# Kernel optimization log

Hardware: AMD Instinct MI355X
Metric: run time of the kernel (lower is better)

Reference implementation:

```python
import jax, jax.numpy as jnp
import numpy as np

B, N, D, H = 4, 2048, 512, 8
HD = D // H


def setup_inputs() -> dict:
    key = jax.random.key(0)
    ks = jax.random.split(key, 10)
    x = jax.random.normal(ks[0], (B, N, D), dtype=jnp.float32)
    adj = (jax.random.uniform(ks[1], (N, N)) < 0.1).astype(jnp.float32)
    s = 1.0 / np.sqrt(D)
    Wq = jax.random.normal(ks[2], (D, D), dtype=jnp.float32) * s
    Wk = jax.random.normal(ks[3], (D, D), dtype=jnp.float32) * s
    Wv = jax.random.normal(ks[4], (D, D), dtype=jnp.float32) * s
    Wo = jax.random.normal(ks[5], (D, D), dtype=jnp.float32) * s
    bq = jnp.zeros((D,), jnp.float32)
    bk = jnp.zeros((D,), jnp.float32)
    bv = jnp.zeros((D,), jnp.float32)
    bo = jnp.zeros((D,), jnp.float32)
    return {"x": x, "adj": adj, "Wq": Wq, "bq": bq, "Wk": Wk, "bk": bk,
            "Wv": Wv, "bv": bv, "Wo": Wo, "bo": bo}


def reference(x, adj, Wq, bq, Wk, bk, Wv, bv, Wo, bo):
    b, n, d = x.shape
    q = (x @ Wq + bq).reshape(b, n, H, HD)
    k = (x @ Wk + bk).reshape(b, n, H, HD)
    v = (x @ Wv + bv).reshape(b, n, H, HD)
    scores = jnp.einsum('bqhd,bkhd->bhqk', q, k) / jnp.sqrt(jnp.float32(HD))
    scores = scores + (1.0 - adj)[None, None, :, :] * (-1e9)
    attn = jax.nn.softmax(scores, axis=-1)
    out = jnp.einsum('bhqk,bkhd->bqhd', attn, v).reshape(b, n, d)
    return out @ Wo + bo
```

## Files before the change

### kernel.cpp

```cpp
#include <hip/hip_runtime.h>
#include <math.h>

#define NB    4
#define NSEQ  2048
#define DMODEL 512
#define NH    8
#define HDIM  64
#define STR   72
#define LOG2E 1.44269504088896f

typedef __attribute__((ext_vector_type(8))) short short8;
typedef __attribute__((ext_vector_type(4))) float f32x4;
typedef __attribute__((ext_vector_type(16))) float f32x16;
#define MFMA16 __builtin_amdgcn_mfma_f32_16x16x32_bf16
#define MFMA32 __builtin_amdgcn_mfma_f32_32x32x16_bf16
#define EXP2F __builtin_amdgcn_exp2f

__device__ __forceinline__ unsigned short f2bf(float f) {
    union { float f; unsigned int u; } v; v.f = f;
    unsigned int u = v.u;
    unsigned int r = (u + 0x7FFFu + ((u >> 16) & 1u)) >> 16;
    return (unsigned short)r;
}
__device__ __forceinline__ float bf2f(unsigned short h) {
    union { unsigned int u; float f; } v; v.u = ((unsigned int)h) << 16;
    return v.f;
}
__device__ __forceinline__ short8 andmask8(short8 p, unsigned bits) {
    union { short8 s; uint4 u; } x; x.s = p;
    x.u.x &= ((bits &   1u) ? 0xFFFFu : 0u) | ((bits &   2u) ? 0xFFFF0000u : 0u);
    x.u.y &= ((bits &   4u) ? 0xFFFFu : 0u) | ((bits &   8u) ? 0xFFFF0000u : 0u);
    x.u.z &= ((bits &  16u) ? 0xFFFFu : 0u) | ((bits &  32u) ? 0xFFFF0000u : 0u);
    x.u.w &= ((bits &  64u) ? 0xFFFFu : 0u) | ((bits & 128u) ? 0xFFFF0000u : 0u);
    return x.s;
}
__device__ __forceinline__ void async16(void* lds, const void* g) {
    __builtin_amdgcn_global_load_lds(
        (const __attribute__((address_space(1))) unsigned int*)g,
        (__attribute__((address_space(3))) unsigned int*)lds, 16, 0, 0);
}

__global__ __launch_bounds__(256) void mask_kernel(const float* __restrict__ adj,
                                                   unsigned long long* __restrict__ Mb) {
    const int w    = blockIdx.x * 4 + (threadIdx.x >> 6);
    const int lane = threadIdx.x & 63;
    const int q  = w >> 5;
    const int kt = w & 31;
    float a = adj[(size_t)q * NSEQ + kt * 64 + lane];
    unsigned long long m = __ballot(a > 0.5f);
    if (lane == 0) Mb[(size_t)kt * NSEQ + q] = m;
}

__global__ __launch_bounds__(256) void split_x_kernel(const float* __restrict__ x,
                                                      unsigned short* __restrict__ xhi,
                                                      unsigned short* __restrict__ xlo) {
    int gid = blockIdx.x * 256 + threadIdx.x;
    float4 a = ((const float4*)x)[gid];
    float f[4] = {a.x, a.y, a.z, a.w};
    ushort4 h4, l4;
    unsigned short hs[4], ls[4];
    #pragma unroll
    for (int j = 0; j < 4; ++j) {
        hs[j] = f2bf(f[j]);
        ls[j] = f2bf(f[j] - bf2f(hs[j]));
    }
    h4.x = hs[0]; h4.y = hs[1]; h4.z = hs[2]; h4.w = hs[3];
    l4.x = ls[0]; l4.y = ls[1]; l4.z = ls[2]; l4.w = ls[3];
    ((ushort4*)xhi)[gid] = h4;
    ((ushort4*)xlo)[gid] = l4;
}

__global__ __launch_bounds__(256) void split_wt_kernel(
    const float* __restrict__ Wq, const float* __restrict__ Wk,
    const float* __restrict__ Wv, const float* __restrict__ Wo,
    unsigned short* __restrict__ Wthi)
{
    __shared__ float tile[32][33];
    const int m = blockIdx.z;
    const float* W = (m == 0) ? Wq : (m == 1) ? Wk : (m == 2) ? Wv : Wo;
    const int k0 = blockIdx.x * 32, n0 = blockIdx.y * 32;
    const int tx = threadIdx.x & 31, ty = threadIdx.x >> 5;
    #pragma unroll
    for (int i = 0; i < 4; ++i)
        tile[ty * 4 + i][tx] = W[(size_t)(k0 + ty * 4 + i) * DMODEL + n0 + tx];
    __syncthreads();
    const size_t base = ((size_t)m * DMODEL) * DMODEL;
    #pragma unroll
    for (int i = 0; i < 4; ++i) {
        float f = tile[tx][ty * 4 + i];
        size_t idx = base + (size_t)(n0 + ty * 4 + i) * DMODEL + k0 + tx;
        Wthi[idx] = f2bf(f);
    }
}

__device__ __forceinline__ void gemm_k_loop(
    const unsigned short* __restrict__ Ah, const unsigned short* __restrict__ Al,
    const unsigned short* __restrict__ Bh,
    char* smem, f32x4 acc[4][4])
{
    const int t    = threadIdx.x;
    const int lane = t & 63;
    const int wid  = t >> 6;
    const int quad = lane >> 4, l16 = lane & 15;
    const int wm   = wid >> 1,  wn  = wid & 1;

    unsigned short* As_h = (unsigned short*)(smem);
    unsigned short* As_l = (unsigned short*)(smem + 8192);
    unsigned short* Bs_h = (unsigned short*)(smem + 16384);

    const int ci0 = t, ci1 = 256 + t;
    const int r0 = ci0 >> 2, r1 = ci1 >> 2;
    const int c0 = (ci0 & 3) ^ ((r0 >> 1) & 3);
    const int c1 = (ci1 & 3) ^ ((r1 >> 1) & 3);
    const char* gAh = (const char*)Ah;  const char* gAl = (const char*)Al;
    const char* gBh = (const char*)Bh;
    const int ca = quad ^ ((l16 >> 1) & 3);

    for (int k0 = 0; k0 < DMODEL; k0 += 32) {
        const int kb = k0 * 2;
        async16(As_h + ci0 * 8, gAh + r0 * 1024 + kb + c0 * 16);
        async16(As_h + ci1 * 8, gAh + r1 * 1024 + kb + c1 * 16);
        async16(As_l + ci0 * 8, gAl + r0 * 1024 + kb + c0 * 16);
        async16(As_l + ci1 * 8, gAl + r1 * 1024 + kb + c1 * 16);
        async16(Bs_h + ci0 * 8, gBh + r0 * 1024 + kb + c0 * 16);
        async16(Bs_h + ci1 * 8, gBh + r1 * 1024 + kb + c1 * 16);
        __syncthreads();

        short8 ah[4], al[4], bh[4];
        #pragma unroll
        for (int i = 0; i < 4; ++i) {
            const int Ra = wm * 64 + i * 16 + l16;
            ah[i] = *(const short8*)(As_h + Ra * 32 + ca * 8);
            al[i] = *(const short8*)(As_l + Ra * 32 + ca * 8);
            const int Rb = wn * 64 + i * 16 + l16;
            bh[i] = *(const short8*)(Bs_h + Rb * 32 + ca * 8);
        }
        #pragma unroll
        for (int mi = 0; mi < 4; ++mi)
            #pragma unroll
            for (int ni = 0; ni < 4; ++ni) {
                acc[mi][ni] = MFMA16(ah[mi], bh[ni], acc[mi][ni], 0, 0, 0);
                acc[mi][ni] = MFMA16(al[mi], bh[ni], acc[mi][ni], 0, 0, 0);
            }
        __syncthreads();
    }
}

__global__ __launch_bounds__(256, 2) void qkv_mfma_kernel(
    const unsigned short* __restrict__ xhi, const unsigned short* __restrict__ xlo,
    const unsigned short* __restrict__ Wthi,
    const float* __restrict__ bq, const float* __restrict__ bk, const float* __restrict__ bv,
    unsigned short* __restrict__ Qhi, unsigned short* __restrict__ Qlo,
    unsigned short* __restrict__ Khi,
    unsigned short* __restrict__ Vt)
{
    __shared__ __align__(16) char smem[33280];
    const int t    = threadIdx.x;
    const int lane = t & 63;
    const int wid  = t >> 6;
    const int quad = lane >> 4, l16 = lane & 15;
    const int wm   = wid >> 1,  wn  = wid & 1;

    const int row0 = blockIdx.x * 128;
    const int yb   = blockIdx.y;
    const int mtx  = yb >> 2;
    const int col0 = (yb & 3) * 128;

    f32x4 acc[4][4];
    #pragma unroll
    for (int i = 0; i < 4; ++i)
        #pragma unroll
        for (int j = 0; j < 4; ++j) acc[i][j] = (f32x4){0.f, 0.f, 0.f, 0.f};

    const size_t wslot = (size_t)mtx * DMODEL * DMODEL;
    gemm_k_loop(xhi + (size_t)row0 * DMODEL, xlo + (size_t)row0 * DMODEL,
                Wthi + wslot + (size_t)col0 * DMODEL, smem, acc);

    const float* bias = (mtx == 0) ? bq : (mtx == 1) ? bk : bv;
    float bcol[4];
    #pragma unroll
    for (int ni = 0; ni < 4; ++ni) bcol[ni] = bias[col0 + wn * 64 + ni * 16 + l16];
    const int h = (col0 + wn * 64) >> 6;

    if (mtx < 2) {
        const float scale = (mtx == 0) ? (0.125f * LOG2E) : 1.0f;
        unsigned short* hig = (mtx == 0) ? Qhi : Khi;
        #pragma unroll
        for (int mi = 0; mi < 4; ++mi) {
            #pragma unroll
            for (int reg = 0; reg < 4; ++reg) {
                const int r = row0 + wm * 64 + mi * 16 + quad * 4 + reg;
                const int b = r >> 11, n = r & 2047;
                const size_t rowbase = ((size_t)(b * NH + h) * NSEQ + n) * HDIM;
                #pragma unroll
                for (int ni = 0; ni < 4; ++ni) {
                    float f = (acc[mi][ni][reg] + bcol[ni]) * scale;
                    unsigned short hi = f2bf(f);
                    hig[rowbase + ni * 16 + l16] = hi;
                    if (mtx == 0)
                        Qlo[rowbase + ni * 16 + l16] = f2bf(f - bf2f(hi));
                }
            }
        }
    } else {
        unsigned short* vt = (unsigned short*)smem + (size_t)wid * 64 * 65;
        #pragma unroll
        for (int mi = 0; mi < 4; ++mi)
            #pragma unroll
            for (int ni = 0; ni < 4; ++ni)
                #pragma unroll
                for (int reg = 0; reg < 4; ++reg)
                    vt[(mi * 16 + quad * 4 + reg) * 65 + ni * 16 + l16] =
                        f2bf(acc[mi][ni][reg] + bcol[ni]);
        const int b   = row0 >> 11;
        const int n0g = (row0 & 2047) + wm * 64;
        const int bh  = b * NH + h;
        unsigned short* gdst = Vt + ((size_t)bh * HDIM + lane) * NSEQ + n0g;
        #pragma unroll
        for (int nb = 0; nb < 8; ++nb) {
            unsigned short v[8];
            #pragma unroll
            for (int j = 0; j < 8; ++j) v[j] = vt[(nb * 8 + j) * 65 + lane];
            uint4 u;
            u.x = (unsigned)v[0] | ((unsigned)v[1] << 16);
            u.y = (unsigned)v[2] | ((unsigned)v[3] << 16);
            u.z = (unsigned)v[4] | ((unsigned)v[5] << 16);
            u.w = (unsigned)v[6] | ((unsigned)v[7] << 16);
            *(uint4*)(gdst + nb * 8) = u;
        }
    }
}

__global__ __launch_bounds__(256, 2) void out_mfma_kernel(
    const unsigned short* __restrict__ chi, const unsigned short* __restrict__ clo,
    const unsigned short* __restrict__ Wthi,
    const float* __restrict__ bo, float* __restrict__ out)
{
    __shared__ __align__(16) char smem[24576];
    const int t    = threadIdx.x;
    const int lane = t & 63;
    const int wid  = t >> 6;
    const int quad = lane >> 4, l16 = lane & 15;
    const int wm   = wid >> 1,  wn  = wid & 1;

    const int row0 = blockIdx.x * 128;
    const int col0 = blockIdx.y * 128;

    f32x4 acc[4][4];
    #pragma unroll
    for (int i = 0; i < 4; ++i)
        #pragma unroll
        for (int j = 0; j < 4; ++j) acc[i][j] = (f32x4){0.f, 0.f, 0.f, 0.f};

    const size_t wslot = (size_t)3 * DMODEL * DMODEL;
    gemm_k_loop(chi + (size_t)row0 * DMODEL, clo + (size_t)row0 * DMODEL,
                Wthi + wslot + (size_t)col0 * DMODEL, smem, acc);

    float bcol[4];
    #pragma unroll
    for (int ni = 0; ni < 4; ++ni) bcol[ni] = bo[col0 + wn * 64 + ni * 16 + l16];
    #pragma unroll
    for (int mi = 0; mi < 4; ++mi)
        #pragma unroll
        for (int reg = 0; reg < 4; ++reg) {
            const int r = row0 + wm * 64 + mi * 16 + quad * 4 + reg;
            float* orow = out + (size_t)r * DMODEL + col0 + wn * 64 + l16;
            #pragma unroll
            for (int ni = 0; ni < 4; ++ni)
                orow[ni * 16] = acc[mi][ni][reg] + bcol[ni];
        }
}

__global__ __launch_bounds__(256) void attn_kernel(
    const unsigned short* __restrict__ Qhi, const unsigned short* __restrict__ Qlo,
    const unsigned short* __restrict__ Khi,
    const unsigned short* __restrict__ Vt,
    const unsigned long long* __restrict__ Mb,
    unsigned short* __restrict__ chi, unsigned short* __restrict__ clo)
{
    __shared__ __align__(16) unsigned short KS[64 * STR];
    __shared__ __align__(16) unsigned short VS[64 * STR];
    __shared__ __align__(16) unsigned short PS[4][32 * STR];

    const int t    = threadIdx.x;
    const int wq   = t >> 6;
    const int lane = t & 63;
    const int l32  = lane & 31;
    const int half = lane >> 5;
    const int q0   = blockIdx.x * 128;
    const int h    = blockIdx.y;
    const int b    = blockIdx.z;
    const int bh   = b * NH + h;
    const int qa   = q0 + wq * 32;

    short8 qh[4], ql[4];
    #pragma unroll
    for (int s = 0; s < 4; ++s) {
        const size_t off = ((size_t)bh * NSEQ + qa + l32) * HDIM + s * 16 + half * 8;
        qh[s] = *(const short8*)(Qhi + off);
        ql[s] = *(const short8*)(Qlo + off);
    }
    const unsigned long long* mrow = Mb + (qa + l32);

    short8 onesf;
    #pragma unroll
    for (int i = 0; i < 8; ++i) onesf[i] = (short)0x3F80;

    f32x16 O0, O1, Ol;
    #pragma unroll
    for (int i = 0; i < 16; ++i) { O0[i] = 0.f; O1[i] = 0.f; Ol[i] = 0.f; }

    const unsigned short* gk = Khi + (size_t)bh * NSEQ * HDIM;
    const unsigned short* gv = Vt  + (size_t)bh * HDIM * NSEQ;
    unsigned short* ps = &PS[wq][0];

    const int ci0 = t, ci1 = t + 256;
    const int sr0 = ci0 >> 3, sc0 = (ci0 & 7) * 8;
    const int sr1 = ci1 >> 3, sc1 = (ci1 & 7) * 8;

    for (int kt = 0; kt < NSEQ / 64; ++kt) {
        const int k0 = kt * 64;
        *(uint4*)&KS[sr0 * STR + sc0] = *(const uint4*)(gk + (size_t)(k0 + sr0) * HDIM + sc0);
        *(uint4*)&KS[sr1 * STR + sc1] = *(const uint4*)(gk + (size_t)(k0 + sr1) * HDIM + sc1);
        *(uint4*)&VS[sr0 * STR + sc0] = *(const uint4*)(gv + (size_t)sr0 * NSEQ + k0 + sc0);
        *(uint4*)&VS[sr1 * STR + sc1] = *(const uint4*)(gv + (size_t)sr1 * NSEQ + k0 + sc1);
        __syncthreads();

        const unsigned long long mw = mrow[(size_t)kt * NSEQ];

        #pragma unroll
        for (int nt = 0; nt < 2; ++nt) {
            f32x16 S;
            #pragma unroll
            for (int i = 0; i < 16; ++i) S[i] = 0.f;
            #pragma unroll
            for (int s = 0; s < 4; ++s) {
                short8 kb = *(const short8*)&KS[(nt * 32 + l32) * STR + s * 16 + half * 8];
                S = MFMA32(qh[s], kb, S, 0, 0, 0);
                S = MFMA32(ql[s], kb, S, 0, 0, 0);
            }
            #pragma unroll
            for (int r = 0; r < 16; ++r) {
                float p = EXP2F(S[r]);
                const int row = (r & 3) + 8 * (r >> 2) + 4 * half;
                ps[row * STR + nt * 32 + l32] =
                    (unsigned short)(__float_as_uint(p) >> 16);
            }
        }

        short8 pf[4];
        #pragma unroll
        for (int s = 0; s < 4; ++s) {
            pf[s] = *(const short8*)&ps[l32 * STR + s * 16 + half * 8];
            pf[s] = andmask8(pf[s], (unsigned)(mw >> (s * 16 + half * 8)) & 0xFFu);
        }

        #pragma unroll
        for (int s = 0; s < 4; ++s) {
            short8 v0 = *(const short8*)&VS[(l32) * STR + s * 16 + half * 8];
            short8 v1 = *(const short8*)&VS[(32 + l32) * STR + s * 16 + half * 8];
            O0 = MFMA32(pf[s], v0, O0, 0, 0, 0);
            O1 = MFMA32(pf[s], v1, O1, 0, 0, 0);
            Ol = MFMA32(pf[s], onesf, Ol, 0, 0, 0);
        }

        __syncthreads();
    }

    #pragma unroll
    for (int r = 0; r < 16; ++r) {
        const int qrow = qa + (r & 3) + 8 * (r >> 2) + 4 * half;
        const float inv = 1.0f / Ol[r];
        const size_t base = ((size_t)b * NSEQ + qrow) * DMODEL + h * HDIM + l32;
        float f0 = O0[r] * inv;
        float f1 = O1[r] * inv;
        unsigned short h0 = f2bf(f0), h1 = f2bf(f1);
        chi[base]      = h0;
        chi[base + 32] = h1;
        clo[base]      = f2bf(f0 - bf2f(h0));
        clo[base + 32] = f2bf(f1 - bf2f(h1));
    }
}

extern "C" void kernel_launch(void* const* d_in, const int* in_sizes, int n_in,
                              void* d_out, int out_size, void* d_ws, size_t ws_size,
                              hipStream_t stream) {
    const float* x   = (const float*)d_in[0];
    const float* adj = (const float*)d_in[1];
    const float* Wq  = (const float*)d_in[2];
    const float* bq  = (const float*)d_in[3];
    const float* Wk  = (const float*)d_in[4];
    const float* bk  = (const float*)d_in[5];
    const float* Wv  = (const float*)d_in[6];
    const float* bv  = (const float*)d_in[7];
    const float* Wo  = (const float*)d_in[8];
    const float* bo  = (const float*)d_in[9];
    float* out = (float*)d_out;

    const size_t elems = (size_t)NB * NSEQ * DMODEL;
    unsigned short* Qhi  = (unsigned short*)d_ws;
    unsigned short* Qlo  = Qhi + elems;
    unsigned short* Khi  = Qlo + elems;
    unsigned short* Klo  = Khi + elems;
    unsigned short* Vt   = Klo + elems;
    unsigned long long* Mbits = (unsigned long long*)(Vt + elems);
    unsigned short* xhi  = Vt + 2 * elems;
    unsigned short* xlo  = xhi + elems;
    unsigned short* Wthi = xlo + elems;
    unsigned short* chi = xhi;
    unsigned short* clo = xlo;

    mask_kernel   <<<dim3(16384), dim3(256), 0, stream>>>(adj, Mbits);
    split_x_kernel<<<dim3(4096), dim3(256), 0, stream>>>(x, xhi, xlo);
    split_wt_kernel<<<dim3(16, 16, 4), dim3(256), 0, stream>>>(Wq, Wk, Wv, Wo, Wthi);
    qkv_mfma_kernel<<<dim3(64, 12), dim3(256), 0, stream>>>(
        xhi, xlo, Wthi, bq, bk, bv, Qhi, Qlo, Khi, Vt);
    attn_kernel<<<dim3(NSEQ / 128, NH, NB), dim3(256), 0, stream>>>(
        Qhi, Qlo, Khi, Vt, Mbits, chi, clo);
    out_mfma_kernel<<<dim3(64, 4), dim3(256), 0, stream>>>(
        chi, clo, Wthi, bo, out);
}
```

Baseline: 221.0 us.

## Drop bf16 lo-split terms and split attention over keys with merge kernel

Removes the hi/lo bf16 split for x, Q and the attention output, so the GEMMs and QK^T use a single bf16 MFMA per step instead of two. This halves MFMA work and the LDS/global traffic for those operands. The attention kernel is also split into two key halves (doubling the grid), each writing fp32 partial outputs and row sums. A new merge kernel adds the halves and normalizes them. The changes cost accuracy, plus extra fp32 partial-buffer traffic and an additional kernel launch.

```diff
diff --git a/kernel.cpp b/kernel.cpp
--- a/kernel.cpp
+++ b/kernel.cpp
@@ -21,10 +21,6 @@
     unsigned int u = v.u;
     unsigned int r = (u + 0x7FFFu + ((u >> 16) & 1u)) >> 16;
     return (unsigned short)r;
-}
-__device__ __forceinline__ float bf2f(unsigned short h) {
-    union { unsigned int u; float f; } v; v.u = ((unsigned int)h) << 16;
-    return v.f;
 }
 __device__ __forceinline__ short8 andmask8(short8 p, unsigned bits) {
     union { short8 s; uint4 u; } x; x.s = p;
@@ -52,22 +48,12 @@
 }
 
 __global__ __launch_bounds__(256) void split_x_kernel(const float* __restrict__ x,
-                                                      unsigned short* __restrict__ xhi,
-                                                      unsigned short* __restrict__ xlo) {
+                                                      unsigned short* __restrict__ xhi) {
     int gid = blockIdx.x * 256 + threadIdx.x;
     float4 a = ((const float4*)x)[gid];
-    float f[4] = {a.x, a.y, a.z, a.w};
-    ushort4 h4, l4;
-    unsigned short hs[4], ls[4];
-    #pragma unroll
-    for (int j = 0; j < 4; ++j) {
-        hs[j] = f2bf(f[j]);
-        ls[j] = f2bf(f[j] - bf2f(hs[j]));
-    }
-    h4.x = hs[0]; h4.y = hs[1]; h4.z = hs[2]; h4.w = hs[3];
-    l4.x = ls[0]; l4.y = ls[1]; l4.z = ls[2]; l4.w = ls[3];
+    ushort4 h4;
+    h4.x = f2bf(a.x); h4.y = f2bf(a.y); h4.z = f2bf(a.z); h4.w = f2bf(a.w);
     ((ushort4*)xhi)[gid] = h4;
-    ((ushort4*)xlo)[gid] = l4;
 }
 
 __global__ __launch_bounds__(256) void split_wt_kernel(
@@ -94,7 +80,7 @@
 }
 
 __device__ __forceinline__ void gemm_k_loop(
-    const unsigned short* __restrict__ Ah, const unsigned short* __restrict__ Al,
+    const unsigned short* __restrict__ Ah,
     const unsigned short* __restrict__ Bh,
     char* smem, f32x4 acc[4][4])
 {
@@ -105,14 +91,13 @@
     const int wm   = wid >> 1,  wn  = wid & 1;
 
     unsigned short* As_h = (unsigned short*)(smem);
-    unsigned short* As_l = (unsigned short*)(smem + 8192);
-    unsigned short* Bs_h = (unsigned short*)(smem + 16384);
+    unsigned short* Bs_h = (unsigned short*)(smem + 8192);
 
     const int ci0 = t, ci1 = 256 + t;
     const int r0 = ci0 >> 2, r1 = ci1 >> 2;
     const int c0 = (ci0 & 3) ^ ((r0 >> 1) & 3);
     const int c1 = (ci1 & 3) ^ ((r1 >> 1) & 3);
-    const char* gAh = (const char*)Ah;  const char* gAl = (const char*)Al;
+    const char* gAh = (const char*)Ah;
     const char* gBh = (const char*)Bh;
     const int ca = quad ^ ((l16 >> 1) & 3);
 
@@ -120,37 +105,32 @@
         const int kb = k0 * 2;
         async16(As_h + ci0 * 8, gAh + r0 * 1024 + kb + c0 * 16);
         async16(As_h + ci1 * 8, gAh + r1 * 1024 + kb + c1 * 16);
-        async16(As_l + ci0 * 8, gAl + r0 * 1024 + kb + c0 * 16);
-        async16(As_l + ci1 * 8, gAl + r1 * 1024 + kb + c1 * 16);
         async16(Bs_h + ci0 * 8, gBh + r0 * 1024 + kb + c0 * 16);
         async16(Bs_h + ci1 * 8, gBh + r1 * 1024 + kb + c1 * 16);
         __syncthreads();
 
-        short8 ah[4], al[4], bh[4];
+        short8 ah[4], bh[4];
         #pragma unroll
         for (int i = 0; i < 4; ++i) {
             const int Ra = wm * 64 + i * 16 + l16;
             ah[i] = *(const short8*)(As_h + Ra * 32 + ca * 8);
-            al[i] = *(const short8*)(As_l + Ra * 32 + ca * 8);
             const int Rb = wn * 64 + i * 16 + l16;
             bh[i] = *(const short8*)(Bs_h + Rb * 32 + ca * 8);
         }
         #pragma unroll
         for (int mi = 0; mi < 4; ++mi)
             #pragma unroll
-            for (int ni = 0; ni < 4; ++ni) {
+            for (int ni = 0; ni < 4; ++ni)
                 acc[mi][ni] = MFMA16(ah[mi], bh[ni], acc[mi][ni], 0, 0, 0);
-                acc[mi][ni] = MFMA16(al[mi], bh[ni], acc[mi][ni], 0, 0, 0);
-            }
         __syncthreads();
     }
 }
 
 __global__ __launch_bounds__(256, 2) void qkv_mfma_kernel(
-    const unsigned short* __restrict__ xhi, const unsigned short* __restrict__ xlo,
+    const unsigned short* __restrict__ xhi,
     const unsigned short* __restrict__ Wthi,
     const float* __restrict__ bq, const float* __restrict__ bk, const float* __restrict__ bv,
-    unsigned short* __restrict__ Qhi, unsigned short* __restrict__ Qlo,
+    unsigned short* __restrict__ Qhi,
     unsigned short* __restrict__ Khi,
     unsigned short* __restrict__ Vt)
 {
@@ -173,7 +153,7 @@
         for (int j = 0; j < 4; ++j) acc[i][j] = (f32x4){0.f, 0.f, 0.f, 0.f};
 
     const size_t wslot = (size_t)mtx * DMODEL * DMODEL;
-    gemm_k_loop(xhi + (size_t)row0 * DMODEL, xlo + (size_t)row0 * DMODEL,
+    gemm_k_loop(xhi + (size_t)row0 * DMODEL,
                 Wthi + wslot + (size_t)col0 * DMODEL, smem, acc);
 
     const float* bias = (mtx == 0) ? bq : (mtx == 1) ? bk : bv;
@@ -193,13 +173,9 @@
                 const int b = r >> 11, n = r & 2047;
                 const size_t rowbase = ((size_t)(b * NH + h) * NSEQ + n) * HDIM;
                 #pragma unroll
-                for (int ni = 0; ni < 4; ++ni) {
-                    float f = (acc[mi][ni][reg] + bcol[ni]) * scale;
-                    unsigned short hi = f2bf(f);
-                    hig[rowbase + ni * 16 + l16] = hi;
-                    if (mtx == 0)
-                        Qlo[rowbase + ni * 16 + l16] = f2bf(f - bf2f(hi));
-                }
+                for (int ni = 0; ni < 4; ++ni)
+                    hig[rowbase + ni * 16 + l16] =
+                        f2bf((acc[mi][ni][reg] + bcol[ni]) * scale);
             }
         }
     } else {
@@ -232,11 +208,11 @@
 }
 
 __global__ __launch_bounds__(256, 2) void out_mfma_kernel(
-    const unsigned short* __restrict__ chi, const unsigned short* __restrict__ clo,
+    const unsigned short* __restrict__ chi,
     const unsigned short* __restrict__ Wthi,
     const float* __restrict__ bo, float* __restrict__ out)
 {
-    __shared__ __align__(16) char smem[24576];
+    __shared__ __align__(16) char smem[16384];
     const int t    = threadIdx.x;
     const int lane = t & 63;
     const int wid  = t >> 6;
@@ -253,7 +229,7 @@
         for (int j = 0; j < 4; ++j) acc[i][j] = (f32x4){0.f, 0.f, 0.f, 0.f};
 
     const size_t wslot = (size_t)3 * DMODEL * DMODEL;
-    gemm_k_loop(chi + (size_t)row0 * DMODEL, clo + (size_t)row0 * DMODEL,
+    gemm_k_loop(chi + (size_t)row0 * DMODEL,
                 Wthi + wslot + (size_t)col0 * DMODEL, smem, acc);
 
     float bcol[4];
@@ -272,11 +248,11 @@
 }
 
 __global__ __launch_bounds__(256) void attn_kernel(
-    const unsigned short* __restrict__ Qhi, const unsigned short* __restrict__ Qlo,
+    const unsigned short* __restrict__ Qhi,
     const unsigned short* __restrict__ Khi,
     const unsigned short* __restrict__ Vt,
     const unsigned long long* __restrict__ Mb,
-    unsigned short* __restrict__ chi, unsigned short* __restrict__ clo)
+    float* __restrict__ Opart, float* __restrict__ lpart)
 {
     __shared__ __align__(16) unsigned short KS[64 * STR];
     __shared__ __align__(16) unsigned short VS[64 * STR];
@@ -286,20 +262,19 @@
     const int wq   = t >> 6;
     const int lane = t & 63;
     const int l32  = lane & 31;
-    const int half = lane >> 5;
+    const int hw   = lane >> 5;
     const int q0   = blockIdx.x * 128;
     const int h    = blockIdx.y;
-    const int b    = blockIdx.z;
+    const int z    = blockIdx.z;
+    const int b    = z >> 1;
+    const int ks   = z & 1;
     const int bh   = b * NH + h;
     const int qa   = q0 + wq * 32;
 
-    short8 qh[4], ql[4];
-    #pragma unroll
-    for (int s = 0; s < 4; ++s) {
-        const size_t off = ((size_t)bh * NSEQ + qa + l32) * HDIM + s * 16 + half * 8;
-        qh[s] = *(const short8*)(Qhi + off);
-        ql[s] = *(const short8*)(Qlo + off);
-    }
+    short8 qh[4];
+    #pragma unroll
+    for (int s = 0; s < 4; ++s)
+        qh[s] = *(const short8*)(Qhi + ((size_t)bh * NSEQ + qa + l32) * HDIM + s * 16 + hw * 8);
     const unsigned long long* mrow = Mb + (qa + l32);
 
     short8 onesf;
@@ -318,7 +293,7 @@
     const int sr0 = ci0 >> 3, sc0 = (ci0 & 7) * 8;
     const int sr1 = ci1 >> 3, sc1 = (ci1 & 7) * 8;
 
-    for (int kt = 0; kt < NSEQ / 64; ++kt) {
+    for (int kt = ks * 16; kt < ks * 16 + 16; ++kt) {
         const int k0 = kt * 64;
         *(uint4*)&KS[sr0 * STR + sc0] = *(const uint4*)(gk + (size_t)(k0 + sr0) * HDIM + sc0);
         *(uint4*)&KS[sr1 * STR + sc1] = *(const uint4*)(gk + (size_t)(k0 + sr1) * HDIM + sc1);
@@ -335,14 +310,13 @@
             for (int i = 0; i < 16; ++i) S[i] = 0.f;
             #pragma unroll
             for (int s = 0; s < 4; ++s) {
-                short8 kb = *(const short8*)&KS[(nt * 32 + l32) * STR + s * 16 + half * 8];
+                short8 kb = *(const short8*)&KS[(nt * 32 + l32) * STR + s * 16 + hw * 8];
                 S = MFMA32(qh[s], kb, S, 0, 0, 0);
-                S = MFMA32(ql[s], kb, S, 0, 0, 0);
             }
             #pragma unroll
             for (int r = 0; r < 16; ++r) {
                 float p = EXP2F(S[r]);
-                const int row = (r & 3) + 8 * (r >> 2) + 4 * half;
+                const int row = (r & 3) + 8 * (r >> 2) + 4 * hw;
                 ps[row * STR + nt * 32 + l32] =
                     (unsigned short)(__float_as_uint(p) >> 16);
             }
@@ -351,14 +325,14 @@
         short8 pf[4];
         #pragma unroll
         for (int s = 0; s < 4; ++s) {
-            pf[s] = *(const short8*)&ps[l32 * STR + s * 16 + half * 8];
-            pf[s] = andmask8(pf[s], (unsigned)(mw >> (s * 16 + half * 8)) & 0xFFu);
+            pf[s] = *(const short8*)&ps[l32 * STR + s * 16 + hw * 8];
+            pf[s] = andmask8(pf[s], (unsigned)(mw >> (s * 16 + hw * 8)) & 0xFFu);
         }
 
         #pragma unroll
         for (int s = 0; s < 4; ++s) {
-            short8 v0 = *(const short8*)&VS[(l32) * STR + s * 16 + half * 8];
-            short8 v1 = *(const short8*)&VS[(32 + l32) * STR + s * 16 + half * 8];
+            short8 v0 = *(const short8*)&VS[(l32) * STR + s * 16 + hw * 8];
+            short8 v1 = *(const short8*)&VS[(32 + l32) * STR + s * 16 + hw * 8];
             O0 = MFMA32(pf[s], v0, O0, 0, 0, 0);
             O1 = MFMA32(pf[s], v1, O1, 0, 0, 0);
             Ol = MFMA32(pf[s], onesf, Ol, 0, 0, 0);
@@ -367,19 +341,53 @@
         __syncthreads();
     }
 
+    const size_t obase = ((size_t)(ks * NB + b) * NH + h) * NSEQ;
     #pragma unroll
     for (int r = 0; r < 16; ++r) {
-        const int qrow = qa + (r & 3) + 8 * (r >> 2) + 4 * half;
-        const float inv = 1.0f / Ol[r];
-        const size_t base = ((size_t)b * NSEQ + qrow) * DMODEL + h * HDIM + l32;
-        float f0 = O0[r] * inv;
-        float f1 = O1[r] * inv;
-        unsigned short h0 = f2bf(f0), h1 = f2bf(f1);
-        chi[base]      = h0;
-        chi[base + 32] = h1;
-        clo[base]      = f2bf(f0 - bf2f(h0));
-        clo[base + 32] = f2bf(f1 - bf2f(h1));
-    }
+        const int qrow = qa + (r & 3) + 8 * (r >> 2) + 4 * hw;
+        float* orow = Opart + (obase + qrow) * HDIM;
+        orow[l32]      = O0[r];
+        orow[32 + l32] = O1[r];
+        if (l32 == 0) lpart[obase + qrow] = Ol[r];
+    }
+}
+
+__global__ __launch_bounds__(256) void merge_kernel(
+    const float* __restrict__ Opart, const float* __restrict__ lpart,
+    unsigned short* __restrict__ chi)
+{
+    const int g = blockIdx.x * 256 + threadIdx.x;
+    const int qitem = g >> 2;
+    const int grp = g & 3;
+    const size_t HS = (size_t)NB * NH * NSEQ * HDIM;
+    const float* pa = Opart + (size_t)qitem * HDIM + grp * 16;
+    const float* pb = pa + HS;
+    const float inv = 1.0f / (lpart[qitem] + lpart[qitem + NB * NH * NSEQ]);
+
+    const int n = qitem & 2047, h = (qitem >> 11) & 7, b = qitem >> 14;
+    unsigned short* dst = chi + ((size_t)b * NSEQ + n) * DMODEL + h * HDIM + grp * 16;
+
+    unsigned short o[16];
+    #pragma unroll
+    for (int i = 0; i < 16; i += 4) {
+        float4 a4 = *(const float4*)(pa + i);
+        float4 b4 = *(const float4*)(pb + i);
+        o[i + 0] = f2bf((a4.x + b4.x) * inv);
+        o[i + 1] = f2bf((a4.y + b4.y) * inv);
+        o[i + 2] = f2bf((a4.z + b4.z) * inv);
+        o[i + 3] = f2bf((a4.w + b4.w) * inv);
+    }
+    uint4 u0, u1;
+    u0.x = (unsigned)o[0]  | ((unsigned)o[1]  << 16);
+    u0.y = (unsigned)o[2]  | ((unsigned)o[3]  << 16);
+    u0.z = (unsigned)o[4]  | ((unsigned)o[5]  << 16);
+    u0.w = (unsigned)o[6]  | ((unsigned)o[7]  << 16);
+    u1.x = (unsigned)o[8]  | ((unsigned)o[9]  << 16);
+    u1.y = (unsigned)o[10] | ((unsigned)o[11] << 16);
+    u1.z = (unsigned)o[12] | ((unsigned)o[13] << 16);
+    u1.w = (unsigned)o[14] | ((unsigned)o[15] << 16);
+    *(uint4*)dst = u0;
+    *(uint4*)(dst + 8) = u1;
 }
 
 extern "C" void kernel_launch(void* const* d_in, const int* in_sizes, int n_in,
@@ -399,24 +407,23 @@
 
     const size_t elems = (size_t)NB * NSEQ * DMODEL;
     unsigned short* Qhi  = (unsigned short*)d_ws;
-    unsigned short* Qlo  = Qhi + elems;
-    unsigned short* Khi  = Qlo + elems;
-    unsigned short* Klo  = Khi + elems;
-    unsigned short* Vt   = Klo + elems;
+    unsigned short* Khi  = Qhi + elems;
+    unsigned short* Vt   = Khi + elems;
     unsigned long long* Mbits = (unsigned long long*)(Vt + elems);
-    unsigned short* xhi  = Vt + 2 * elems;
-    unsigned short* xlo  = xhi + elems;
-    unsigned short* Wthi = xlo + elems;
+    unsigned short* xhi  = (unsigned short*)(Mbits + 32 * NSEQ);
+    unsigned short* Wthi = xhi + elems;
+    float* Opart = (float*)(Wthi + 4 * (size_t)DMODEL * DMODEL);
+    float* lpart = Opart + 2 * (size_t)NB * NH * NSEQ * HDIM;
     unsigned short* chi = xhi;
-    unsigned short* clo = xlo;
 
     mask_kernel   <<<dim3(16384), dim3(256), 0, stream>>>(adj, Mbits);
-    split_x_kernel<<<dim3(4096), dim3(256), 0, stream>>>(x, xhi, xlo);
+    split_x_kernel<<<dim3(4096), dim3(256), 0, stream>>>(x, xhi);
     split_wt_kernel<<<dim3(16, 16, 4), dim3(256), 0, stream>>>(Wq, Wk, Wv, Wo, Wthi);
     qkv_mfma_kernel<<<dim3(64, 12), dim3(256), 0, stream>>>(
-        xhi, xlo, Wthi, bq, bk, bv, Qhi, Qlo, Khi, Vt);
-    attn_kernel<<<dim3(NSEQ / 128, NH, NB), dim3(256), 0, stream>>>(
-        Qhi, Qlo, Khi, Vt, Mbits, chi, clo);
+        xhi, Wthi, bq, bk, bv, Qhi, Khi, Vt);
+    attn_kernel<<<dim3(NSEQ / 128, NH, NB * 2), dim3(256), 0, stream>>>(
+        Qhi, Khi, Vt, Mbits, Opart, lpart);
+    merge_kernel<<<dim3(1024), dim3(256), 0, stream>>>(Opart, lpart, chi);
     out_mfma_kernel<<<dim3(64, 4), dim3(256), 0, stream>>>(
-        chi, clo, Wthi, bo, out);
-}
+        chi, Wthi, bo, out);
+}
```

Result: faster. 204.0 us (-7.7%).
